# Kernel optimization log

Hardware: AMD Instinct MI355X
Metric: run time of the kernel (lower is better)

## Reference

```python
import jax, jax.numpy as jnp
import numpy as np
import math

KSIZE = 7
CHANNELS = 256


def setup_inputs() -> dict:
    key = jax.random.key(0)
    k1, k2, k3, k4 = jax.random.split(key, 4)
    B, C, H, W = 8, CHANNELS, 256, 256
    x = jax.random.normal(k1, (B, C, H, W), dtype=jnp.float32)
    # torch defaults: log_sigma = log(1)=0, log_freq = log(0.2), theta = 0; add small noise
    log_sigma = 0.0 + 0.05 * jax.random.normal(k2, (C,), dtype=jnp.float32)
    log_freq = jnp.float32(math.log(0.2)) + 0.05 * jax.random.normal(k3, (C,), dtype=jnp.float32)
    theta = 0.05 * jax.random.normal(k4, (C,), dtype=jnp.float32)
    return {"x": x, "log_sigma": log_sigma, "log_freq": log_freq, "theta": theta}


def _gabor_kernels(log_sigma, log_freq, theta, dtype):
    """Vectorized per-channel Gabor kernel synthesis. Returns [C, 1, k, k]."""
    half = KSIZE // 2
    r = jnp.arange(-half, half + 1, dtype=dtype)
    gx, gy = jnp.meshgrid(r, r, indexing="ij")  # [k, k]
    sigma = jnp.exp(log_sigma)[:, None, None]   # [C,1,1]
    freq = jnp.exp(log_freq)[:, None, None]
    c = jnp.cos(theta)[:, None, None]
    s = jnp.sin(theta)[:, None, None]
    # xy = grid @ rot.T / sigma, with rot = [[c, s], [-s, c]] so rot.T = [[c, -s], [s, c]]
    x0 = (gx[None] * c + gy[None] * s) / sigma    # [C,k,k]
    x1 = (-gx[None] * s + gy[None] * c) / sigma   # [C,k,k]
    gauss = jnp.exp(-(x0 * x0 + x1 * x1) / 2)
    kern = gauss * jnp.cos(2 * jnp.pi * freq * x0)
    kern = kern / jnp.sum(kern, axis=(1, 2), keepdims=True)
    return kern[:, None]  # [C,1,k,k]


def reference(x, log_sigma, log_freq, theta):
    C = x.shape[1]
    weight = _gabor_kernels(log_sigma, log_freq, theta, x.dtype)
    pad = KSIZE // 2
    # depthwise conv (groups=C); NOTE: original forward omits stride, so stride=1
    out = jax.lax.conv_general_dilated(
        x, weight,
        window_strides=(1, 1),
        padding=[(pad, pad), (pad, pad)],
        dimension_numbers=("NCHW", "OIHW", "NCHW"),
        feature_group_count=C,
    )
    return out
```

## Files before the change

### kernel.cpp

```cpp
#include <hip/hip_runtime.h>
#include <math.h>

#define KSIZE 7
#define C_CH  256
#define HW    256
#define BATCH 8

#define TH    32
#define ROWS  (TH + 6)
#define LDW   264

__global__ void gabor_weights_kernel(const float* __restrict__ log_sigma,
                                     const float* __restrict__ log_freq,
                                     const float* __restrict__ theta,
                                     float* __restrict__ gw) {
    int c = threadIdx.x;
    if (c >= C_CH) return;
    float sigma = expf(log_sigma[c]);
    float freq  = expf(log_freq[c]);
    float ct = cosf(theta[c]);
    float st = sinf(theta[c]);
    float inv_sigma = 1.0f / sigma;
    float vals[KSIZE * KSIZE];
    float sum = 0.0f;
    #pragma unroll
    for (int i = 0; i < KSIZE; ++i) {
        #pragma unroll
        for (int j = 0; j < KSIZE; ++j) {
            float dx = (float)(i - 3);
            float dy = (float)(j - 3);
            float x0 = (dx * ct + dy * st) * inv_sigma;
            float x1 = (-dx * st + dy * ct) * inv_sigma;
            float g  = expf(-0.5f * (x0 * x0 + x1 * x1));
            float v  = g * cosf(6.283185307179586f * freq * x0);
            vals[i * KSIZE + j] = v;
            sum += v;
        }
    }
    float inv = 1.0f / sum;
    #pragma unroll
    for (int k = 0; k < KSIZE * KSIZE; ++k)
        gw[c * (KSIZE * KSIZE) + k] = vals[k] * inv;
}

__global__ __launch_bounds__(256, 4)
void gabor_conv_kernel(const float* __restrict__ x,
                       const float* __restrict__ gw,
                       float* __restrict__ out) {
    __shared__ float tile[ROWS][LDW];

    const int tid = threadIdx.x;
    const int ht  = blockIdx.x;
    const int c   = blockIdx.y;
    const int n   = blockIdx.z;

    const size_t plane = ((size_t)n * C_CH + c) * (size_t)(HW * HW);
    const float* xp = x + plane;
    float*       op = out + plane;
    const int row0 = ht * TH - 3;

    const int NF4 = ROWS * (LDW / 4);
    for (int idx = tid; idx < NF4; idx += 256) {
        int rr = idx / 66;
        int q  = idx - rr * 66;
        float4 v = make_float4(0.f, 0.f, 0.f, 0.f);
        int gr = row0 + rr;
        if (q >= 1 && q <= 64 && gr >= 0 && gr < HW) {
            v = *reinterpret_cast<const float4*>(xp + (size_t)gr * HW + (q - 1) * 4);
        }
        *reinterpret_cast<float4*>(&tile[rr][q * 4]) = v;
    }

    float w[KSIZE * KSIZE];
    const float* wp = gw + c * (KSIZE * KSIZE);
    #pragma unroll
    for (int k = 0; k < KSIZE * KSIZE; ++k) w[k] = wp[k];

    __syncthreads();

    const int wq   = tid & 63;
    const int rg   = tid >> 6;
    const int ob   = rg * 8;
    const int colp = wq * 4;

    float acc[8][4];
    #pragma unroll
    for (int o = 0; o < 8; ++o)
        #pragma unroll
        for (int cc = 0; cc < 4; ++cc) acc[o][cc] = 0.f;

    #pragma unroll
    for (int r = 0; r < 14; ++r) {
        float4 a = *reinterpret_cast<const float4*>(&tile[ob + r][colp]);
        float4 b = *reinterpret_cast<const float4*>(&tile[ob + r][colp + 4]);
        float4 d = *reinterpret_cast<const float4*>(&tile[ob + r][colp + 8]);
        float f[12] = {a.x, a.y, a.z, a.w, b.x, b.y, b.z, b.w, d.x, d.y, d.z, d.w};
        #pragma unroll
        for (int o = 0; o < 8; ++o) {
            if (o <= r && r <= o + 6) {
                const int ki = r - o;
                #pragma unroll
                for (int cc = 0; cc < 4; ++cc) {
                    #pragma unroll
                    for (int j = 0; j < KSIZE; ++j)
                        acc[o][cc] += f[cc + j + 1] * w[ki * KSIZE + j];
                }
            }
        }
    }

    const int orow0 = ht * TH + ob;
    #pragma unroll
    for (int o = 0; o < 8; ++o) {
        float4 v = make_float4(acc[o][0], acc[o][1], acc[o][2], acc[o][3]);
        *reinterpret_cast<float4*>(op + (size_t)(orow0 + o) * HW + wq * 4) = v;
    }
}

extern "C" void kernel_launch(void* const* d_in, const int* in_sizes, int n_in,
                              void* d_out, int out_size, void* d_ws, size_t ws_size,
                              hipStream_t stream) {
    const float* x  = (const float*)d_in[0];
    const float* ls = (const float*)d_in[1];
    const float* lf = (const float*)d_in[2];
    const float* th = (const float*)d_in[3];
    float* out = (float*)d_out;
    float* gw  = (float*)d_ws;

    gabor_weights_kernel<<<1, 256, 0, stream>>>(ls, lf, th, gw);

    dim3 grid(HW / TH, C_CH, BATCH);
    gabor_conv_kernel<<<grid, 256, 0, stream>>>(x, gw, out);
}
```

Before: 296.0 us.

## Make conv blocks persistent per plane with double-buffered async global-to-LDS loads

Each block now owns a whole (batch, channel) plane instead of one 32-row tile. It walks the eight row tiles in a loop, prefetching the next tile into a second LDS buffer with global_load_lds while computing the current one. The aim is to overlap global loads with the FMA work and to drop per-tile block launch overhead and the per-thread staging through registers. In exchange it uses twice the LDS per block, which lowers occupancy to two blocks per CU and cuts the number of blocks from 16384 to 2048. That may leave fewer memory requests in flight for what is mainly a bandwidth-bound kernel.

Result: faster. 282.0 us (-4.7%).

```diff
diff --git a/kernel.cpp b/kernel.cpp
--- a/kernel.cpp
+++ b/kernel.cpp
@@ -9,6 +9,7 @@
 #define TH    32
 #define ROWS  (TH + 6)
 #define LDW   264
+#define NT    (HW / TH)
 
 __global__ void gabor_weights_kernel(const float* __restrict__ log_sigma,
                                      const float* __restrict__ log_freq,
@@ -43,32 +44,34 @@
         gw[c * (KSIZE * KSIZE) + k] = vals[k] * inv;
 }
 
-__global__ __launch_bounds__(256, 4)
+__device__ __forceinline__ void gload_lds16(const float* g, float* l) {
+    __builtin_amdgcn_global_load_lds(
+        (const __attribute__((address_space(1))) void*)g,
+        (__attribute__((address_space(3))) void*)l,
+        16, 0, 0);
+}
+
+__global__ __launch_bounds__(256, 2)
 void gabor_conv_kernel(const float* __restrict__ x,
                        const float* __restrict__ gw,
                        float* __restrict__ out) {
-    __shared__ float tile[ROWS][LDW];
+    __shared__ float tile[2][ROWS][LDW];
 
-    const int tid = threadIdx.x;
-    const int ht  = blockIdx.x;
-    const int c   = blockIdx.y;
-    const int n   = blockIdx.z;
+    const int tid  = threadIdx.x;
+    const int lane = tid & 63;
+    const int wv   = tid >> 6;
+    const int c    = blockIdx.x;
+    const int n    = blockIdx.y;
 
     const size_t plane = ((size_t)n * C_CH + c) * (size_t)(HW * HW);
     const float* xp = x + plane;
     float*       op = out + plane;
-    const int row0 = ht * TH - 3;
 
-    const int NF4 = ROWS * (LDW / 4);
-    for (int idx = tid; idx < NF4; idx += 256) {
-        int rr = idx / 66;
-        int q  = idx - rr * 66;
-        float4 v = make_float4(0.f, 0.f, 0.f, 0.f);
-        int gr = row0 + rr;
-        if (q >= 1 && q <= 64 && gr >= 0 && gr < HW) {
-            v = *reinterpret_cast<const float4*>(xp + (size_t)gr * HW + (q - 1) * 4);
-        }
-        *reinterpret_cast<float4*>(&tile[rr][q * 4]) = v;
+    for (int idx = tid; idx < 2 * ROWS; idx += 256) {
+        int b  = idx / ROWS;
+        int rr = idx - b * ROWS;
+        *reinterpret_cast<float4*>(&tile[b][rr][0])   = make_float4(0.f, 0.f, 0.f, 0.f);
+        *reinterpret_cast<float4*>(&tile[b][rr][260]) = make_float4(0.f, 0.f, 0.f, 0.f);
     }
 
     float w[KSIZE * KSIZE];
@@ -76,45 +79,67 @@
     #pragma unroll
     for (int k = 0; k < KSIZE * KSIZE; ++k) w[k] = wp[k];
 
+#define STAGE(BUF, T) do {                                                   \
+        const int row0_ = (T) * TH - 3;                                      \
+        for (int rr = wv; rr < ROWS; rr += 4) {                              \
+            int gr = row0_ + rr;                                             \
+            if (gr >= 0 && gr < HW) {                                        \
+                gload_lds16(xp + (size_t)gr * HW + lane * 4,                 \
+                            &tile[BUF][rr][4]);                              \
+            } else {                                                         \
+                *reinterpret_cast<float4*>(&tile[BUF][rr][4 + lane * 4]) =   \
+                    make_float4(0.f, 0.f, 0.f, 0.f);                         \
+            }                                                                \
+        }                                                                    \
+    } while (0)
+
+    STAGE(0, 0);
     __syncthreads();
 
-    const int wq   = tid & 63;
-    const int rg   = tid >> 6;
-    const int ob   = rg * 8;
-    const int colp = wq * 4;
+    const int colp = lane * 4;
+    const int ob   = wv * 8;
 
-    float acc[8][4];
-    #pragma unroll
-    for (int o = 0; o < 8; ++o)
+    for (int t = 0; t < NT; ++t) {
+        const int cur = t & 1;
+
+        if (t + 1 < NT) STAGE(cur ^ 1, t + 1);
+
+        float acc[8][4];
         #pragma unroll
-        for (int cc = 0; cc < 4; ++cc) acc[o][cc] = 0.f;
+        for (int o = 0; o < 8; ++o)
+            #pragma unroll
+            for (int cc = 0; cc < 4; ++cc) acc[o][cc] = 0.f;
 
-    #pragma unroll
-    for (int r = 0; r < 14; ++r) {
-        float4 a = *reinterpret_cast<const float4*>(&tile[ob + r][colp]);
-        float4 b = *reinterpret_cast<const float4*>(&tile[ob + r][colp + 4]);
-        float4 d = *reinterpret_cast<const float4*>(&tile[ob + r][colp + 8]);
-        float f[12] = {a.x, a.y, a.z, a.w, b.x, b.y, b.z, b.w, d.x, d.y, d.z, d.w};
         #pragma unroll
-        for (int o = 0; o < 8; ++o) {
-            if (o <= r && r <= o + 6) {
-                const int ki = r - o;
-                #pragma unroll
-                for (int cc = 0; cc < 4; ++cc) {
+        for (int r = 0; r < 14; ++r) {
+            float4 a = *reinterpret_cast<const float4*>(&tile[cur][ob + r][colp]);
+            float4 b = *reinterpret_cast<const float4*>(&tile[cur][ob + r][colp + 4]);
+            float4 d = *reinterpret_cast<const float4*>(&tile[cur][ob + r][colp + 8]);
+            float f[12] = {a.x, a.y, a.z, a.w, b.x, b.y, b.z, b.w, d.x, d.y, d.z, d.w};
+            #pragma unroll
+            for (int o = 0; o < 8; ++o) {
+                if (o <= r && r <= o + 6) {
+                    const int ki = r - o;
                     #pragma unroll
-                    for (int j = 0; j < KSIZE; ++j)
-                        acc[o][cc] += f[cc + j + 1] * w[ki * KSIZE + j];
+                    for (int cc = 0; cc < 4; ++cc) {
+                        #pragma unroll
+                        for (int j = 0; j < KSIZE; ++j)
+                            acc[o][cc] += f[cc + j + 1] * w[ki * KSIZE + j];
+                    }
                 }
             }
         }
+
+        const int orow0 = t * TH + ob;
+        #pragma unroll
+        for (int o = 0; o < 8; ++o) {
+            float4 v = make_float4(acc[o][0], acc[o][1], acc[o][2], acc[o][3]);
+            *reinterpret_cast<float4*>(op + (size_t)(orow0 + o) * HW + colp) = v;
+        }
+
+        __syncthreads();
     }
-
-    const int orow0 = ht * TH + ob;
-    #pragma unroll
-    for (int o = 0; o < 8; ++o) {
-        float4 v = make_float4(acc[o][0], acc[o][1], acc[o][2], acc[o][3]);
-        *reinterpret_cast<float4*>(op + (size_t)(orow0 + o) * HW + wq * 4) = v;
-    }
+#undef STAGE
 }
 
 extern "C" void kernel_launch(void* const* d_in, const int* in_sizes, int n_in,
@@ -129,6 +154,6 @@
 
     gabor_weights_kernel<<<1, 256, 0, stream>>>(ls, lf, th, gw);
 
-    dim3 grid(HW / TH, C_CH, BATCH);
+    dim3 grid(C_CH, BATCH);
     gabor_conv_kernel<<<grid, 256, 0, stream>>>(x, gw, out);
 }
```
